# Performance work log

Measured on AMD Instinct MI355X. Metric: run time of the kernel, lower is better.

Reference implementation:

```python
import jax, jax.numpy as jnp
import numpy as np
import math

D_MODEL = 1024
N_HEADS = 16
D_HEAD = D_MODEL // N_HEADS


def setup_inputs() -> dict:
    key = jax.random.key(0)
    k_x, k_wqkv, k_bqkv, k_wp, k_bp = jax.random.split(key, 5)
    B, T = 2, 2048
    s = 1.0 / math.sqrt(D_MODEL)
    return {
        "x": jax.random.normal(k_x, (B, T, D_MODEL), dtype=jnp.float32),
        "W_qkv": jax.random.uniform(k_wqkv, (D_MODEL, 3 * D_MODEL), minval=-s, maxval=s, dtype=jnp.float32),
        "b_qkv": jax.random.uniform(k_bqkv, (3 * D_MODEL,), minval=-s, maxval=s, dtype=jnp.float32),
        "W_proj": jax.random.uniform(k_wp, (D_MODEL, D_MODEL), minval=-s, maxval=s, dtype=jnp.float32),
        "b_proj": jax.random.uniform(k_bp, (D_MODEL,), minval=-s, maxval=s, dtype=jnp.float32),
    }


def reference(x, W_qkv, b_qkv, W_proj, b_proj):
    B, T, C = x.shape
    qkv = x @ W_qkv + b_qkv                      # [B,T,3C]
    qkv = qkv.reshape(B, T, 3, N_HEADS, D_HEAD)
    qkv = jnp.transpose(qkv, (2, 0, 3, 1, 4))     # [3,B,H,T,dh]
    q, k, v = qkv[0], qkv[1], qkv[2]
    scale = math.sqrt(D_HEAD)
    attn = jnp.einsum('bhqd,bhkd->bhqk', q, k) / scale  # [B,H,T,T]
    causal = jnp.tril(jnp.ones((T, T), dtype=bool))
    attn = jnp.where(causal, attn, -jnp.inf)
    attn = jax.nn.softmax(attn, axis=-1)
    out = jnp.einsum('bhqk,bhkd->bhqd', attn, v)  # [B,H,T,dh]
    out = jnp.transpose(out, (0, 2, 1, 3)).reshape(B, T, C)
    return out @ W_proj + b_proj
```

## Files before the change

kernel.cpp:

```cpp
#include <hip/hip_runtime.h>

#define B_    2
#define T_    2048
#define C_    1024
#define H_    16
#define DH_   64
#define M_    (B_ * T_)
#define NQKV  (3 * C_)

typedef __bf16 bf16;
typedef __bf16 bf16x4 __attribute__((ext_vector_type(4)));
typedef __bf16 bf16x8 __attribute__((ext_vector_type(8)));
typedef float  f32x4  __attribute__((ext_vector_type(4)));

__device__ __forceinline__ void async16(const void* g, void* l) {
  __builtin_amdgcn_global_load_lds(
      (const __attribute__((address_space(1))) void*)g,
      (__attribute__((address_space(3))) void*)l, 16, 0, 0);
}

__global__ __launch_bounds__(256) void prep_k(
    const float* __restrict__ x, bf16* __restrict__ xbf,
    const float* __restrict__ Wqkv, bf16* __restrict__ wqkvT,
    const float* __restrict__ Wproj, bf16* __restrict__ wprojT) {
  __shared__ float tile[32][33];
  const int bid = blockIdx.x;
  if (bid < 4096) {
    const int i = (bid * 256 + threadIdx.x) * 4;
    float4 v = *(const float4*)(x + i);
    bf16x4 o;
    o[0] = (bf16)v.x; o[1] = (bf16)v.y; o[2] = (bf16)v.z; o[3] = (bf16)v.w;
    *(bf16x4*)(xbf + i) = o;
    return;
  }
  const float* in; bf16* out; int R, C, cb, rb;
  if (bid < 4096 + 3072) {
    const int b = bid - 4096;
    in = Wqkv; out = wqkvT; R = 1024; C = 3072; cb = b % 96; rb = b / 96;
  } else {
    const int b = bid - 7168;
    in = Wproj; out = wprojT; R = 1024; C = 1024; cb = b & 31; rb = b >> 5;
  }
  const int c0 = cb * 32, r0 = rb * 32;
  const int tx = threadIdx.x & 31, ty = threadIdx.x >> 5;
#pragma unroll
  for (int j = 0; j < 4; j++)
    tile[ty + j * 8][tx] = in[(size_t)(r0 + ty + j * 8) * C + c0 + tx];
  __syncthreads();
#pragma unroll
  for (int j = 0; j < 4; j++)
    out[(size_t)(c0 + ty + j * 8) * R + r0 + tx] = (bf16)tile[tx][ty + j * 8];
}

template <int EPI, int BM>
__global__ __launch_bounds__(256) void gemm_k(
    const bf16* __restrict__ A, const bf16* __restrict__ Bt,
    const float* __restrict__ bias, float* __restrict__ outF,
    bf16* __restrict__ qb, bf16* __restrict__ kb, bf16* __restrict__ vtb) {
  constexpr int K = 1024;
  constexpr int MI = BM / 32;
  __shared__ alignas(16) bf16 As[BM * 64];
  __shared__ alignas(16) bf16 Bs[128 * 64];
  const int tid = threadIdx.x;
  const int lane = tid & 63, wv = tid >> 6;
  const int l15 = lane & 15, quad = lane >> 4;
  const int wm = (wv >> 1) * (BM / 2), wn = (wv & 1) * 64;
  const int m0 = blockIdx.x * BM, n0 = blockIdx.y * 128;

  f32x4 acc[MI][4] = {};

  const int srow = tid >> 3;
  const int sgb = ((tid & 7) ^ (srow & 7)) * 8;
  const bf16* ga = A + (size_t)(m0 + srow) * K + sgb;
  const bf16* gb = Bt + (size_t)(n0 + srow) * K + sgb;
  const int swz = l15 & 7;

  for (int it = 0; it < K / 64; ++it) {
    const int k0 = it * 64;
#pragma unroll
    for (int c = 0; c < BM / 32; c++)
      async16(ga + k0 + (size_t)(c * 32) * K, As + tid * 8 + c * 2048);
#pragma unroll
    for (int c = 0; c < 4; c++)
      async16(gb + k0 + (size_t)(c * 32) * K, Bs + tid * 8 + c * 2048);
    __syncthreads();
    bf16x8 af[2][MI], bfr[2][4];
#pragma unroll
    for (int kk = 0; kk < 2; kk++) {
#pragma unroll
      for (int i = 0; i < MI; i++)
        af[kk][i] = *(const bf16x8*)(As + (wm + i * 16 + l15) * 64 +
                                     (((kk * 4 + quad) ^ swz) << 3));
#pragma unroll
      for (int j = 0; j < 4; j++)
        bfr[kk][j] = *(const bf16x8*)(Bs + (wn + j * 16 + l15) * 64 +
                                      (((kk * 4 + quad) ^ swz) << 3));
    }
#pragma unroll
    for (int kk = 0; kk < 2; kk++)
#pragma unroll
      for (int i = 0; i < MI; i++)
#pragma unroll
        for (int j = 0; j < 4; j++)
          acc[i][j] = __builtin_amdgcn_mfma_f32_16x16x32_bf16(
              af[kk][i], bfr[kk][j], acc[i][j], 0, 0, 0);
    __syncthreads();
  }

#pragma unroll
  for (int i = 0; i < MI; i++) {
#pragma unroll
    for (int j = 0; j < 4; j++) {
      const int gcol = n0 + wn + j * 16 + l15;
      const float bv = bias[gcol];
      const int trow = m0 + wm + i * 16 + quad * 4;
      if constexpr (EPI == 0) {
        const int which = gcol >> 10;
        const int hn = gcol & 1023;
        const int h = hn >> 6, d = hn & 63;
        const int bb = trow >> 11, t = trow & 2047;
        const int head = bb * 16 + h;
        if (which == 0) {
#pragma unroll
          for (int r = 0; r < 4; r++)
            qb[head * 131072 + (t + r) * 64 + d] =
                (bf16)((acc[i][j][r] + bv) * 0.1803368801f);
        } else if (which == 1) {
#pragma unroll
          for (int r = 0; r < 4; r++)
            kb[head * 131072 + (t + r) * 64 + d] = (bf16)(acc[i][j][r] + bv);
        } else {
          bf16x4 pv;
#pragma unroll
          for (int r = 0; r < 4; r++) pv[r] = (bf16)(acc[i][j][r] + bv);
          *(bf16x4*)(vtb + head * 131072 + d * 2048 + t) = pv;
        }
      } else {
#pragma unroll
        for (int r = 0; r < 4; r++)
          outF[(size_t)(trow + r) * 1024 + gcol] = acc[i][j][r] + bv;
      }
    }
  }
}

__global__ __launch_bounds__(512, 4) void attn_k(const bf16* __restrict__ Q,
                                                 const bf16* __restrict__ K,
                                                 const bf16* __restrict__ Vt,
                                                 bf16* __restrict__ O) {
  __shared__ alignas(16) bf16 Ks[128 * 64];
  __shared__ alignas(16) bf16 Vs[2][64 * 128];
  __shared__ alignas(16) bf16 Ps[8][16 * 64];
  const int tid = threadIdx.x, lane = tid & 63, wv = tid >> 6;
  const int l15 = lane & 15, quad = lane >> 4;

  const int b = blockIdx.x;
  const int sH = b >> 8, i = b & 255;
  const int bh = (i & 7) | (((i >> 3) & 3) << 3);
  const int x = i >> 5;
  const int qJ = sH ? (15 - x) : x;
  const int q0 = qJ * 128;
  const int nIter = qJ + 1;

  const bf16* Qb = Q + (size_t)bh * 131072;
  const bf16* Kb = K + (size_t)bh * 131072;
  const bf16* Vb = Vt + (size_t)bh * 131072;

  const int krow = tid >> 3;
  const int kg = (tid & 7) ^ (krow & 7);
  const bf16* gk = Kb + krow * 64 + kg * 8;
  const int vrow = tid >> 4;
  const int vg = (tid & 15) ^ (vrow & 15);
  const bf16* gv = Vb + vrow * 2048 + vg * 8;

  const int swz7 = l15 & 7;
  bf16* Pw = Ps[wv];
  const int bb = bh >> 4, h = bh & 15;

  const int q = q0 + wv * 16 + l15;
  bf16x8 aq0 = *(const bf16x8*)(Qb + q * 64 + quad * 8);
  bf16x8 aq1 = *(const bf16x8*)(Qb + q * 64 + 32 + quad * 8);

  f32x4 o[4] = {};
  float m = -3.0e38f, lsum = 0.f;

  async16(gk, &Ks[tid * 8]);
  async16(gk + 64 * 64, &Ks[tid * 8 + 4096]);
  async16(gv, &Vs[0][tid * 8]);
  async16(gv + 32 * 2048, &Vs[0][tid * 8 + 4096]);

  for (int it = 0; it < nIter; ++it) {
    __syncthreads();
    const bf16* Vc = Vs[it & 1];

    bf16x8 kf0[8], kf1[8];
#pragma unroll
    for (int nf = 0; nf < 8; nf++)
      kf0[nf] = *(const bf16x8*)(Ks + (nf * 16 + l15) * 64 + ((quad ^ swz7) << 3));
#pragma unroll
    for (int nf = 0; nf < 8; nf++)
      kf1[nf] = *(const bf16x8*)(Ks + (nf * 16 + l15) * 64 + (((4 + quad) ^ swz7) << 3));

    f32x4 s[8] = {};
    __builtin_amdgcn_s_setprio(1);
#pragma unroll
    for (int nf = 0; nf < 8; nf++)
      s[nf] = __builtin_amdgcn_mfma_f32_16x16x32_bf16(kf0[nf], aq0, s[nf], 0, 0, 0);
    __builtin_amdgcn_s_setprio(0);

    __syncthreads();
    if (it + 1 < nIter) {
      const int kt1 = (it + 1) * 128;
      async16(gk + kt1 * 64, &Ks[tid * 8]);
      async16(gk + kt1 * 64 + 64 * 64, &Ks[tid * 8 + 4096]);
      async16(gv + kt1, &Vs[(it + 1) & 1][tid * 8]);
      async16(gv + kt1 + 32 * 2048, &Vs[(it + 1) & 1][tid * 8 + 4096]);
    }

    __builtin_amdgcn_s_setprio(1);
#pragma unroll
    for (int nf = 0; nf < 8; nf++)
      s[nf] = __builtin_amdgcn_mfma_f32_16x16x32_bf16(kf1[nf], aq1, s[nf], 0, 0, 0);
    __builtin_amdgcn_s_setprio(0);

    if (it == nIter - 1) {
#pragma unroll
      for (int nf = 0; nf < 8; nf++)
#pragma unroll
        for (int r = 0; r < 4; r++) {
          const int kt = it * 128 + nf * 16 + quad * 4 + r;
          if (kt > q) s[nf][r] = -3.0e38f;
        }
    }

    float mx = s[0][0];
#pragma unroll
    for (int nf = 0; nf < 8; nf++)
#pragma unroll
      for (int r = 0; r < 4; r++) mx = fmaxf(mx, s[nf][r]);
    mx = fmaxf(mx, __shfl_xor(mx, 16));
    mx = fmaxf(mx, __shfl_xor(mx, 32));
    if (!__all(mx - m <= 8.0f)) {
      const float mnew = fmaxf(m, mx);
      const float alpha = __builtin_amdgcn_exp2f(m - mnew);
      m = mnew;
      lsum *= alpha;
#pragma unroll
      for (int nf = 0; nf < 4; nf++)
#pragma unroll
        for (int r = 0; r < 4; r++) o[nf][r] *= alpha;
    }
    float ts = 0.f;
    bf16x4 p4[8];
#pragma unroll
    for (int nf = 0; nf < 8; nf++)
#pragma unroll
      for (int r = 0; r < 4; r++) {
        const float pv = __builtin_amdgcn_exp2f(s[nf][r] - m);
        ts += pv;
        p4[nf][r] = (bf16)pv;
      }
    ts += __shfl_xor(ts, 16);
    ts += __shfl_xor(ts, 32);
    lsum += ts;

#pragma unroll
    for (int half = 0; half < 2; half++) {
#pragma unroll
      for (int nf = 0; nf < 4; nf++)
        *(bf16x4*)(Pw + l15 * 64 + ((((nf << 1) | (quad >> 1)) ^ swz7) << 3) +
                   ((quad & 1) << 2)) = p4[half * 4 + nf];
      bf16x8 pb0 = *(const bf16x8*)(Pw + l15 * 64 + ((quad ^ swz7) << 3));
      bf16x8 pb1 = *(const bf16x8*)(Pw + l15 * 64 + (((4 + quad) ^ swz7) << 3));
      __builtin_amdgcn_s_setprio(1);
#pragma unroll
      for (int kc = 0; kc < 2; kc++) {
        bf16x8 pb = kc ? pb1 : pb0;
        const int kcg = half * 2 + kc;
#pragma unroll
        for (int nf = 0; nf < 4; nf++) {
          bf16x8 vf = *(const bf16x8*)(Vc + (nf * 16 + l15) * 128 +
                                       (((kcg * 4 + quad) ^ l15) << 3));
          o[nf] = __builtin_amdgcn_mfma_f32_16x16x32_bf16(vf, pb, o[nf], 0, 0, 0);
        }
      }
      __builtin_amdgcn_s_setprio(0);
    }
  }

  const float inv = 1.0f / lsum;
#pragma unroll
  for (int nf = 0; nf < 4; nf++) {
    bf16x4 ov;
#pragma unroll
    for (int r = 0; r < 4; r++) ov[r] = (bf16)(o[nf][r] * inv);
    *(bf16x4*)(O + (size_t)(bb * 2048 + q) * 1024 + h * 64 + nf * 16 + quad * 4) = ov;
  }
}

extern "C" void kernel_launch(void* const* d_in, const int* in_sizes, int n_in,
                              void* d_out, int out_size, void* d_ws, size_t ws_size,
                              hipStream_t stream) {
  const float* x     = (const float*)d_in[0];
  const float* Wqkv  = (const float*)d_in[1];
  const float* bqkv  = (const float*)d_in[2];
  const float* Wproj = (const float*)d_in[3];
  const float* bproj = (const float*)d_in[4];
  float* out = (float*)d_out;

  char* p = (char*)d_ws;
  bf16* xbf    = (bf16*)p; p += (size_t)M_ * C_ * 2;
  bf16* wqkvT  = (bf16*)p; p += (size_t)NQKV * C_ * 2;
  bf16* wprojT = (bf16*)p; p += (size_t)C_ * C_ * 2;
  bf16* Qb     = (bf16*)p; p += (size_t)M_ * C_ * 2;
  bf16* Kb     = (bf16*)p; p += (size_t)M_ * C_ * 2;
  bf16* Vtb    = (bf16*)p; p += (size_t)M_ * C_ * 2;
  bf16* AO     = (bf16*)p;

  prep_k<<<8192, 256, 0, stream>>>(x, xbf, Wqkv, wqkvT, Wproj, wprojT);

  gemm_k<0, 64><<<dim3(M_ / 64, NQKV / 128), 256, 0, stream>>>(
      xbf, wqkvT, bqkv, nullptr, Qb, Kb, Vtb);

  attn_k<<<512, 512, 0, stream>>>(Qb, Kb, Vtb, AO);

  gemm_k<1, 64><<<dim3(M_ / 64, C_ / 128), 256, 0, stream>>>(
      AO, wprojT, bproj, out, nullptr, nullptr, nullptr);
}
```

Measured before the change: 173.1 us.

## Switch attention to 32x32x16 MFMA with register-shuffled P and double-buffered K

The attention kernel now uses 4 waves of 256 threads, each owning 32 query rows, and computes QK^T and PV with 32x32x16 bf16 MFMAs instead of 16x16x32. The softmax probabilities are packed to bf16 pairs and rearranged across lanes with a cross-half shuffle, so they feed the PV MFMA directly without the per-wave LDS round trip. K is now double-buffered like V, which removes one barrier per iteration. The changes aim at fewer LDS transactions, fewer syncs and better MFMA efficiency, at the cost of more registers per thread and fewer threads per block.

```diff
diff --git a/kernel.cpp b/kernel.cpp
--- a/kernel.cpp
+++ b/kernel.cpp
@@ -9,14 +9,22 @@
 #define NQKV  (3 * C_)
 
 typedef __bf16 bf16;
+typedef __bf16 bf16x2 __attribute__((ext_vector_type(2)));
 typedef __bf16 bf16x4 __attribute__((ext_vector_type(4)));
 typedef __bf16 bf16x8 __attribute__((ext_vector_type(8)));
 typedef float  f32x4  __attribute__((ext_vector_type(4)));
+typedef float  f32x16 __attribute__((ext_vector_type(16)));
+typedef unsigned u32x4 __attribute__((ext_vector_type(4)));
 
 __device__ __forceinline__ void async16(const void* g, void* l) {
   __builtin_amdgcn_global_load_lds(
       (const __attribute__((address_space(1))) void*)g,
       (__attribute__((address_space(3))) void*)l, 16, 0, 0);
+}
+
+__device__ __forceinline__ unsigned pk(float a, float b) {
+  bf16x2 t; t[0] = (bf16)a; t[1] = (bf16)b;
+  return __builtin_bit_cast(unsigned, t);
 }
 
 __global__ __launch_bounds__(256) void prep_k(
@@ -144,15 +152,14 @@
   }
 }
 
-__global__ __launch_bounds__(512, 4) void attn_k(const bf16* __restrict__ Q,
+__global__ __launch_bounds__(256, 2) void attn_k(const bf16* __restrict__ Q,
                                                  const bf16* __restrict__ K,
                                                  const bf16* __restrict__ Vt,
                                                  bf16* __restrict__ O) {
-  __shared__ alignas(16) bf16 Ks[128 * 64];
+  __shared__ alignas(16) bf16 Ks[2][128 * 64];
   __shared__ alignas(16) bf16 Vs[2][64 * 128];
-  __shared__ alignas(16) bf16 Ps[8][16 * 64];
   const int tid = threadIdx.x, lane = tid & 63, wv = tid >> 6;
-  const int l15 = lane & 15, quad = lane >> 4;
+  const int l31 = lane & 31, hi = lane >> 5;
 
   const int b = blockIdx.x;
   const int sH = b >> 8, i = b & 255;
@@ -173,128 +180,128 @@
   const int vg = (tid & 15) ^ (vrow & 15);
   const bf16* gv = Vb + vrow * 2048 + vg * 8;
 
-  const int swz7 = l15 & 7;
-  bf16* Pw = Ps[wv];
+  const int swzk = l31 & 7;
+  const int swzv = l31 & 15;
   const int bb = bh >> 4, h = bh & 15;
 
-  const int q = q0 + wv * 16 + l15;
-  bf16x8 aq0 = *(const bf16x8*)(Qb + q * 64 + quad * 8);
-  bf16x8 aq1 = *(const bf16x8*)(Qb + q * 64 + 32 + quad * 8);
-
-  f32x4 o[4] = {};
+  const int q = q0 + wv * 32 + l31;
+  bf16x8 aq[4];
+#pragma unroll
+  for (int ds = 0; ds < 4; ds++)
+    aq[ds] = *(const bf16x8*)(Qb + q * 64 + ds * 16 + hi * 8);
+
+  f32x16 o0 = {}, o1 = {};
   float m = -3.0e38f, lsum = 0.f;
 
-  async16(gk, &Ks[tid * 8]);
-  async16(gk + 64 * 64, &Ks[tid * 8 + 4096]);
-  async16(gv, &Vs[0][tid * 8]);
-  async16(gv + 32 * 2048, &Vs[0][tid * 8 + 4096]);
+#pragma unroll
+  for (int c = 0; c < 4; c++) {
+    async16(gk + c * (32 * 64), &Ks[0][tid * 8 + c * 2048]);
+    async16(gv + c * (16 * 2048), &Vs[0][tid * 8 + c * 2048]);
+  }
 
   for (int it = 0; it < nIter; ++it) {
-    __syncthreads();
-    const bf16* Vc = Vs[it & 1];
-
-    bf16x8 kf0[8], kf1[8];
-#pragma unroll
-    for (int nf = 0; nf < 8; nf++)
-      kf0[nf] = *(const bf16x8*)(Ks + (nf * 16 + l15) * 64 + ((quad ^ swz7) << 3));
-#pragma unroll
-    for (int nf = 0; nf < 8; nf++)
-      kf1[nf] = *(const bf16x8*)(Ks + (nf * 16 + l15) * 64 + (((4 + quad) ^ swz7) << 3));
-
-    f32x4 s[8] = {};
-    __builtin_amdgcn_s_setprio(1);
-#pragma unroll
-    for (int nf = 0; nf < 8; nf++)
-      s[nf] = __builtin_amdgcn_mfma_f32_16x16x32_bf16(kf0[nf], aq0, s[nf], 0, 0, 0);
-    __builtin_amdgcn_s_setprio(0);
-
+    const int cur = it & 1;
     __syncthreads();
     if (it + 1 < nIter) {
       const int kt1 = (it + 1) * 128;
-      async16(gk + kt1 * 64, &Ks[tid * 8]);
-      async16(gk + kt1 * 64 + 64 * 64, &Ks[tid * 8 + 4096]);
-      async16(gv + kt1, &Vs[(it + 1) & 1][tid * 8]);
-      async16(gv + kt1 + 32 * 2048, &Vs[(it + 1) & 1][tid * 8 + 4096]);
-    }
-
+#pragma unroll
+      for (int c = 0; c < 4; c++) {
+        async16(gk + kt1 * 64 + c * (32 * 64), &Ks[cur ^ 1][tid * 8 + c * 2048]);
+        async16(gv + kt1 + c * (16 * 2048), &Vs[cur ^ 1][tid * 8 + c * 2048]);
+      }
+    }
+    const bf16* Kc = Ks[cur];
+    const bf16* Vc = Vs[cur];
+
+    f32x16 s[4] = {};
     __builtin_amdgcn_s_setprio(1);
 #pragma unroll
-    for (int nf = 0; nf < 8; nf++)
-      s[nf] = __builtin_amdgcn_mfma_f32_16x16x32_bf16(kf1[nf], aq1, s[nf], 0, 0, 0);
+    for (int nf = 0; nf < 4; nf++) {
+      const int row = nf * 32 + l31;
+#pragma unroll
+      for (int ds = 0; ds < 4; ds++) {
+        bf16x8 kf = *(const bf16x8*)(Kc + row * 64 + (((ds * 2 + hi) ^ swzk) << 3));
+        s[nf] = __builtin_amdgcn_mfma_f32_32x32x16_bf16(kf, aq[ds], s[nf], 0, 0, 0);
+      }
+    }
     __builtin_amdgcn_s_setprio(0);
 
     if (it == nIter - 1) {
 #pragma unroll
-      for (int nf = 0; nf < 8; nf++)
-#pragma unroll
-        for (int r = 0; r < 4; r++) {
-          const int kt = it * 128 + nf * 16 + quad * 4 + r;
+      for (int nf = 0; nf < 4; nf++)
+#pragma unroll
+        for (int r = 0; r < 16; r++) {
+          const int kt = it * 128 + nf * 32 + (r & 3) + 8 * (r >> 2) + 4 * hi;
           if (kt > q) s[nf][r] = -3.0e38f;
         }
     }
 
     float mx = s[0][0];
 #pragma unroll
-    for (int nf = 0; nf < 8; nf++)
-#pragma unroll
-      for (int r = 0; r < 4; r++) mx = fmaxf(mx, s[nf][r]);
-    mx = fmaxf(mx, __shfl_xor(mx, 16));
+    for (int nf = 0; nf < 4; nf++)
+#pragma unroll
+      for (int r = 0; r < 16; r++) mx = fmaxf(mx, s[nf][r]);
     mx = fmaxf(mx, __shfl_xor(mx, 32));
     if (!__all(mx - m <= 8.0f)) {
       const float mnew = fmaxf(m, mx);
       const float alpha = __builtin_amdgcn_exp2f(m - mnew);
-      m = mnew;
-      lsum *= alpha;
-#pragma unroll
-      for (int nf = 0; nf < 4; nf++)
-#pragma unroll
-        for (int r = 0; r < 4; r++) o[nf][r] *= alpha;
+      m = mnew; lsum *= alpha;
+#pragma unroll
+      for (int r = 0; r < 16; r++) { o0[r] *= alpha; o1[r] *= alpha; }
     }
     float ts = 0.f;
-    bf16x4 p4[8];
-#pragma unroll
-    for (int nf = 0; nf < 8; nf++)
-#pragma unroll
-      for (int r = 0; r < 4; r++) {
-        const float pv = __builtin_amdgcn_exp2f(s[nf][r] - m);
-        ts += pv;
-        p4[nf][r] = (bf16)pv;
-      }
-    ts += __shfl_xor(ts, 16);
+    unsigned w[4][8];
+#pragma unroll
+    for (int nf = 0; nf < 4; nf++)
+#pragma unroll
+      for (int k = 0; k < 8; k++) {
+        const float pa = __builtin_amdgcn_exp2f(s[nf][2 * k] - m);
+        const float pc = __builtin_amdgcn_exp2f(s[nf][2 * k + 1] - m);
+        ts += pa + pc;
+        w[nf][k] = pk(pa, pc);
+      }
     ts += __shfl_xor(ts, 32);
     lsum += ts;
 
-#pragma unroll
-    for (int half = 0; half < 2; half++) {
-#pragma unroll
-      for (int nf = 0; nf < 4; nf++)
-        *(bf16x4*)(Pw + l15 * 64 + ((((nf << 1) | (quad >> 1)) ^ swz7) << 3) +
-                   ((quad & 1) << 2)) = p4[half * 4 + nf];
-      bf16x8 pb0 = *(const bf16x8*)(Pw + l15 * 64 + ((quad ^ swz7) << 3));
-      bf16x8 pb1 = *(const bf16x8*)(Pw + l15 * 64 + (((4 + quad) ^ swz7) << 3));
-      __builtin_amdgcn_s_setprio(1);
-#pragma unroll
-      for (int kc = 0; kc < 2; kc++) {
-        bf16x8 pb = kc ? pb1 : pb0;
-        const int kcg = half * 2 + kc;
-#pragma unroll
-        for (int nf = 0; nf < 4; nf++) {
-          bf16x8 vf = *(const bf16x8*)(Vc + (nf * 16 + l15) * 128 +
-                                       (((kcg * 4 + quad) ^ l15) << 3));
-          o[nf] = __builtin_amdgcn_mfma_f32_16x16x32_bf16(vf, pb, o[nf], 0, 0, 0);
-        }
-      }
-      __builtin_amdgcn_s_setprio(0);
-    }
+    __builtin_amdgcn_s_setprio(1);
+#pragma unroll
+    for (int nf = 0; nf < 4; nf++) {
+#pragma unroll
+      for (int half = 0; half < 2; half++) {
+        const unsigned w0 = w[nf][half * 4 + 0], w1 = w[nf][half * 4 + 1];
+        const unsigned w2 = w[nf][half * 4 + 2], w3 = w[nf][half * 4 + 3];
+        const unsigned rx = (unsigned)__shfl_xor((int)(hi ? w0 : w2), 32);
+        const unsigned ry = (unsigned)__shfl_xor((int)(hi ? w1 : w3), 32);
+        u32x4 pw;
+        pw[0] = hi ? rx : w0;
+        pw[1] = hi ? ry : w1;
+        pw[2] = hi ? w2 : rx;
+        pw[3] = hi ? w3 : ry;
+        const bf16x8 pb = __builtin_bit_cast(bf16x8, pw);
+        const int c = nf * 2 + half;
+        const bf16x8 vf0 = *(const bf16x8*)(Vc + l31 * 128 +
+                                            (((c * 2 + hi) ^ swzv) << 3));
+        o0 = __builtin_amdgcn_mfma_f32_32x32x16_bf16(vf0, pb, o0, 0, 0, 0);
+        const bf16x8 vf1 = *(const bf16x8*)(Vc + (32 + l31) * 128 +
+                                            (((c * 2 + hi) ^ swzv) << 3));
+        o1 = __builtin_amdgcn_mfma_f32_32x32x16_bf16(vf1, pb, o1, 0, 0, 0);
+      }
+    }
+    __builtin_amdgcn_s_setprio(0);
   }
 
   const float inv = 1.0f / lsum;
-#pragma unroll
-  for (int nf = 0; nf < 4; nf++) {
-    bf16x4 ov;
-#pragma unroll
-    for (int r = 0; r < 4; r++) ov[r] = (bf16)(o[nf][r] * inv);
-    *(bf16x4*)(O + (size_t)(bb * 2048 + q) * 1024 + h * 64 + nf * 16 + quad * 4) = ov;
+  bf16* Op = O + (size_t)(bb * 2048 + q) * 1024 + h * 64;
+#pragma unroll
+  for (int g = 0; g < 4; g++) {
+    bf16x4 v0, v1;
+#pragma unroll
+    for (int k = 0; k < 4; k++) {
+      v0[k] = (bf16)(o0[g * 4 + k] * inv);
+      v1[k] = (bf16)(o1[g * 4 + k] * inv);
+    }
+    *(bf16x4*)(Op + g * 8 + hi * 4) = v0;
+    *(bf16x4*)(Op + 32 + g * 8 + hi * 4) = v1;
   }
 }
 
@@ -322,7 +329,7 @@
   gemm_k<0, 64><<<dim3(M_ / 64, NQKV / 128), 256, 0, stream>>>(
       xbf, wqkvT, bqkv, nullptr, Qb, Kb, Vtb);
 
-  attn_k<<<512, 512, 0, stream>>>(Qb, Kb, Vtb, AO);
+  attn_k<<<512, 256, 0, stream>>>(Qb, Kb, Vtb, AO);
 
   gemm_k<1, 64><<<dim3(M_ / 64, C_ / 128), 256, 0, stream>>>(
       AO, wprojT, bproj, out, nullptr, nullptr, nullptr);
```

Measured after the change: 173.6 us. No clear change (+0.3%).
